# Kernel optimization log

Hardware: AMD Instinct MI355X
Metric: run time of the kernel (lower is better)

The kernel has to match this reference:

```python
import jax, jax.numpy as jnp
import numpy as np

KLD_SCALE = 10.0
COMMIT_COST = 0.25


def setup_inputs() -> dict:
    key = jax.random.key(0)
    k1, k2, k3, k4 = jax.random.split(key, 4)
    B, C, T = 32, 512, 4096
    D, K = 128, 1024
    z = jax.random.normal(k1, (B, C, T), dtype=jnp.float32)
    proj_w = jax.random.normal(k2, (D, C), dtype=jnp.float32) * (1.0 / np.sqrt(C))
    proj_b = jax.random.normal(k3, (D,), dtype=jnp.float32) * 0.01
    embed_w = jax.random.normal(k4, (K, D), dtype=jnp.float32)
    return {"z": z, "proj_w": proj_w, "proj_b": proj_b, "embed_w": embed_w}


def reference(z, proj_w, proj_b, embed_w):
    B, C, T = z.shape
    D = proj_w.shape[0]
    # 1x1 Conv1d == per-timestep linear: [B,C,T] x [D,C] -> [B,T,D]
    z_e = jnp.einsum('bct,dc->btd', z, proj_w) + proj_b
    flat = z_e.reshape(-1, D)  # [B*T, D]
    # squared euclidean distances to codebook: [B*T, K]
    dist = (jnp.sum(flat * flat, axis=1, keepdims=True)
            - 2.0 * (flat @ embed_w.T)
            + jnp.sum(embed_w * embed_w, axis=1)[None, :])
    ind = jnp.argmin(dist, axis=1).reshape(B, T)  # == argmax(-dist)
    z_q = embed_w[ind]  # [B,T,D] codebook gather
    sg = jax.lax.stop_gradient
    diff = KLD_SCALE * (COMMIT_COST * jnp.mean((sg(z_q) - z_e) ** 2)
                        + jnp.mean((z_q - sg(z_e)) ** 2))
    z_q_ste = z_e + sg(z_q - z_e)  # straight-through estimator
    z_q_out = jnp.transpose(z_q_ste, (0, 2, 1))  # [B,D,T]
    return z_q_out, diff, ind
```

## Files before the change

kernel.cpp:

```cpp
#include <hip/hip_runtime.h>

#define B_N 32
#define C_N 512
#define T_N 4096
#define D_N 128
#define K_N 1024
#define N_N (B_N * T_N)

typedef _Float16 f16x8 __attribute__((ext_vector_type(8)));
typedef float    f32x4 __attribute__((ext_vector_type(4)));

#define ZSWZ_OFF 0
#define ESWZ_OFF 67108864
#define ENS_OFF  67895296
#define IND_OFF  67899392
#define PART_OFF 68423680
#define WSWZ_OFF 68431872

#define GLL(g, s) __builtin_amdgcn_global_load_lds( \
    (const __attribute__((address_space(1))) unsigned int*)(g), \
    (__attribute__((address_space(3))) unsigned int*)(s), 16, 0, 0)

__global__ __launch_bounds__(128) void k_eprep(const float* __restrict__ E,
                                               _Float16* __restrict__ eswz,
                                               float* __restrict__ ens) {
  __shared__ float s2[2];
  const int code = blockIdx.x, d = threadIdx.x;
  const float e  = E[(size_t)code * D_N + d];
  const float es = e * 64.f;
  const _Float16 eh = (_Float16)es;
  const _Float16 el = (_Float16)(es - (float)eh);

  float sq = es * es;
  #pragma unroll
  for (int off = 32; off > 0; off >>= 1) sq += __shfl_down(sq, off);
  if ((d & 63) == 0) s2[d >> 6] = sq;
  __syncthreads();
  if (d == 0) ens[code] = s2[0] + s2[1];

  const int kt = code >> 7, mi = (code >> 4) & 7, lrow = code & 15;
  const int lk = (d >> 3) & 3, i = d & 7, cb = d >> 5;
  const size_t tile = (size_t)kt * 12;
  #define PUT(c, v) eswz[(((tile + (c)) * 512 + mi * 64 + lk * 16 + lrow) << 3) + i] = (v)
  PUT(cb, eh);
  PUT(4 + cb, el);
  PUT(8 + cb, eh);
  #undef PUT
}

__global__ __launch_bounds__(256) void k_wprep(const float* __restrict__ W,
                                               _Float16* __restrict__ wswz) {
  const int e = blockIdx.x * 256 + threadIdx.x;
  const int d = e >> 9, c = e & 511;
  const float x = W[d * C_N + c] * 8.f;
  const _Float16 h  = (_Float16)x;
  const _Float16 lo = (_Float16)(x - (float)h);
  const int kc = c >> 5, gg = (c >> 3) & 3, j = c & 7;
  const int nf = d >> 4, ll = gg * 16 + (d & 15);
  const size_t base = (size_t)kc * 8192 + ((size_t)nf * 64 + ll) * 8 + j;
  wswz[base]        = h;
  wswz[base + 4096] = lo;
}

__global__ __launch_bounds__(256, 2) void k_projm(const float* __restrict__ z,
                                                  const _Float16* __restrict__ wswz,
                                                  const float* __restrict__ bias,
                                                  f16x8* __restrict__ zswz) {
  __shared__ __align__(16) char lds[65536];

  const int tid = threadIdx.x;
  const int l   = tid & 63, w = tid >> 6;
  const int g   = l >> 4, li = l & 15;
  const int b   = blockIdx.y, t0 = blockIdx.x * 128;
  const float* zb = z + (size_t)b * C_N * T_N + t0;

  float bs[8];
  #pragma unroll
  for (int nf = 0; nf < 8; ++nf) bs[nf] = bias[nf * 16 + li] * 64.f;

  f32x4 acc[2][8];
  #pragma unroll
  for (int mi = 0; mi < 2; ++mi)
    #pragma unroll
    for (int nf = 0; nf < 8; ++nf) acc[mi][nf] = (f32x4)0.f;

  auto stage = [&](int kc, int buf) {
    char* zdst = lds + buf * 16384;
    char* wdst = lds + 32768 + buf * 16384;
    #pragma unroll
    for (int s = 0; s < 4; ++s) {
      const int q = w * 4 + s;
      const unsigned v = q * 64 + l;
      const unsigned u = v ^ (((v >> 8) & 1) << 2);
      GLL((const char*)zb +
              ((size_t)(kc * 32 + (u >> 5)) * T_N + (size_t)(u & 31) * 4) * 4,
          zdst + q * 1024);
      GLL((const char*)wswz + (size_t)kc * 16384 + q * 1024 + l * 16,
          wdst + q * 1024);
    }
  };

  stage(0, 0);
  __syncthreads();

  int buf = 0;
  for (int kc = 0; kc < 16; ++kc) {
    if (kc + 1 < 16) stage(kc + 1, buf ^ 1);

    const float* zl = (const float*)(lds + buf * 16384);
    const f16x8* wb = (const f16x8*)(lds + 32768 + buf * 16384);

    f16x8 ah[2], al[2];
    #pragma unroll
    for (int mi = 0; mi < 2; ++mi) {
      const int mt = w * 2 + mi;
      const int a0 = (g * 1024 + mt * 16 + li) ^ ((g & 1) << 4);
      #pragma unroll
      for (int j = 0; j < 8; ++j) {
        const float x = zl[a0 + j * 128] * 8.f;
        const _Float16 h = (_Float16)x;
        ah[mi][j] = h;
        al[mi][j] = (_Float16)(x - (float)h);
      }
    }
    f16x8 bh[8], bl[8];
    #pragma unroll
    for (int nf = 0; nf < 8; ++nf) {
      bh[nf] = wb[nf * 64 + l];
      bl[nf] = wb[512 + nf * 64 + l];
    }
    #pragma unroll
    for (int mi = 0; mi < 2; ++mi)
      #pragma unroll
      for (int nf = 0; nf < 8; ++nf) {
        acc[mi][nf] = __builtin_amdgcn_mfma_f32_16x16x32_f16(ah[mi], bh[nf], acc[mi][nf], 0, 0, 0);
        acc[mi][nf] = __builtin_amdgcn_mfma_f32_16x16x32_f16(al[mi], bh[nf], acc[mi][nf], 0, 0, 0);
        acc[mi][nf] = __builtin_amdgcn_mfma_f32_16x16x32_f16(ah[mi], bl[nf], acc[mi][nf], 0, 0, 0);
      }
    __syncthreads();
    buf ^= 1;
  }

  unsigned* cs = (unsigned*)lds;
  const int n0 = b * T_N + t0;
  for (int p = 0; p < 2; ++p) {
    #pragma unroll
    for (int mi = 0; mi < 2; ++mi) {
      const int trow = (w * 2 + mi) * 16 + g * 4;
      #pragma unroll
      for (int nfl = 0; nfl < 4; ++nfl) {
        const int nf = p * 4 + nfl;
        #pragma unroll
        for (int r = 0; r < 4; ++r) {
          const float x = acc[mi][nf][r] + bs[nf];
          const _Float16 h  = (_Float16)x;
          const _Float16 lo = (_Float16)(x - (float)h);
          cs[(trow + r) * 68 + nfl * 16 + li] =
              (unsigned)__builtin_bit_cast(unsigned short, h) |
              ((unsigned)__builtin_bit_cast(unsigned short, lo) << 16);
        }
      }
    }
    __syncthreads();
    #pragma unroll
    for (int i = 0; i < 4; ++i) {
      const int u = i * 256 + tid;
      const int t = u & 127, dc = u >> 7;
      f16x8 vh, vl;
      #pragma unroll
      for (int e = 0; e < 8; ++e) {
        const unsigned vv = cs[t * 68 + dc * 8 + e];
        vh[e] = __builtin_bit_cast(_Float16, (unsigned short)(vv & 0xffff));
        vl[e] = __builtin_bit_cast(_Float16, (unsigned short)(vv >> 16));
      }
      const int n = n0 + t;
      const int cu = p * 2 + (dc >> 2), lk = dc & 3;
      const size_t idx = ((size_t)(n >> 4) * 8 + cu) * 64 + lk * 16 + (n & 15);
      zswz[idx]       = vh;
      zswz[idx + 256] = vl;
    }
    __syncthreads();
  }
}

__global__ __launch_bounds__(256) void k_argmin(const f16x8* __restrict__ zswz,
                                                const f16x8* __restrict__ eswz,
                                                const float* __restrict__ ens,
                                                int* __restrict__ ind,
                                                float* __restrict__ indf) {
  __shared__ f16x8 rows[4096];
  __shared__ f16x8 abuf[2][512];

  const int tid = threadIdx.x;
  const int l   = tid & 63, w = tid >> 6;
  const int wr  = w >> 1, wc = w & 1;
  const int blk = blockIdx.x;

  const char* zsrc = (const char*)zswz + (size_t)blk * 65536;
  #pragma unroll
  for (int s = 0; s < 16; ++s)
    GLL(zsrc + s * 4096 + tid * 16, &rows[s * 256 + w * 64]);

  {
    const char* asrc = (const char*)eswz;
    GLL(asrc + tid * 16,        &abuf[0][w * 64]);
    GLL(asrc + 4096 + tid * 16, &abuf[0][256 + w * 64]);
  }
  __syncthreads();

  float bestd[4];
  int   bestk[4];
  #pragma unroll
  for (int nf = 0; nf < 4; ++nf) { bestd[nf] = 3.4e38f; bestk[nf] = 0; }

  int buf = 0;
  for (int kt = 0; kt < 8; ++kt) {
    f32x4 acc[4][4];
    #pragma unroll
    for (int mi = 0; mi < 4; ++mi)
      #pragma unroll
      for (int nf = 0; nf < 4; ++nf) acc[mi][nf] = (f32x4)0.f;

    for (int c = 0; c < 12; ++c) {
      int nkt = kt, nc = c + 1;
      if (nc == 12) { nc = 0; ++nkt; }
      if (nkt < 8) {
        const char* asrc = (const char*)eswz + ((size_t)(nkt * 12 + nc) * 512) * 16;
        GLL(asrc + tid * 16,        &abuf[buf ^ 1][w * 64]);
        GLL(asrc + 4096 + tid * 16, &abuf[buf ^ 1][256 + w * 64]);
      }
      const int cu = (c < 8) ? (c & 3) : (c - 4);
      f16x8 bfr[4], afr[4];
      #pragma unroll
      for (int nf = 0; nf < 4; ++nf)
        bfr[nf] = rows[((wc * 4 + nf) * 8 + cu) * 64 + l];
      #pragma unroll
      for (int mi = 0; mi < 4; ++mi)
        afr[mi] = abuf[buf][(wr * 4 + mi) * 64 + l];
      #pragma unroll
      for (int mi = 0; mi < 4; ++mi)
        #pragma unroll
        for (int nf = 0; nf < 4; ++nf)
          acc[mi][nf] = __builtin_amdgcn_mfma_f32_16x16x32_f16(
              afr[mi], bfr[nf], acc[mi][nf], 0, 0, 0);
      __syncthreads();
      buf ^= 1;
    }

    #pragma unroll
    for (int mi = 0; mi < 4; ++mi) {
      const int cbase = kt * 128 + wr * 64 + mi * 16 + ((l >> 4) << 2);
      const float4 e4 = *(const float4*)&ens[cbase];
      const float ev[4] = {e4.x, e4.y, e4.z, e4.w};
      #pragma unroll
      for (int r = 0; r < 4; ++r) {
        const int k = cbase + r;
        #pragma unroll
        for (int nf = 0; nf < 4; ++nf) {
          const float dv = ev[r] - 2.0f * acc[mi][nf][r];
          if (dv < bestd[nf]) { bestd[nf] = dv; bestk[nf] = k; }
        }
      }
    }
  }

  float* sd = (float*)&rows[0];
  int*   sk = (int*)((float*)&rows[0] + 256);
  #pragma unroll
  for (int nf = 0; nf < 4; ++nf) {
    float d = bestd[nf]; int k = bestk[nf];
    #pragma unroll
    for (int off = 16; off < 64; off <<= 1) {
      const float od = __shfl_xor(d, off);
      const int   ok = __shfl_xor(k, off);
      if (od < d || (od == d && ok < k)) { d = od; k = ok; }
    }
    if (l < 16) {
      sd[wr * 128 + wc * 64 + nf * 16 + l] = d;
      sk[wr * 128 + wc * 64 + nf * 16 + l] = k;
    }
  }
  __syncthreads();
  if (tid < 128) {
    float d0 = sd[tid], d1 = sd[128 + tid];
    int   k0 = sk[tid], k1 = sk[128 + tid];
    if (d1 < d0 || (d1 == d0 && k1 < k0)) { d0 = d1; k0 = k1; }
    const int n = blk * 128 + tid;
    ind[n]  = k0;
    indf[n] = (float)k0;
  }
}

__global__ __launch_bounds__(256) void k_out(const f16x8* __restrict__ zswz,
                                             const float* __restrict__ E,
                                             const int* __restrict__ ind,
                                             float* __restrict__ out,
                                             float* __restrict__ part) {
  __shared__ float es[64][129];
  __shared__ int   si[64];
  __shared__ float wsum[4];

  const int b   = blockIdx.y;
  const int t0  = blockIdx.x * 64;
  const int tid = threadIdx.x;

  if (tid < 64) si[tid] = ind[b * T_N + t0 + tid];
  __syncthreads();

  float psum = 0.f;
  const int n0 = b * T_N + t0;
  #pragma unroll
  for (int u = tid; u < 1024; u += 256) {
    const int t = u >> 4, db = u & 15;
    const int n = n0 + t;
    const size_t base = ((size_t)(n >> 4) * 8 + (db >> 2)) * 64 + (db & 3) * 16 + (n & 15);
    const f16x8 vh = zswz[base];
    const f16x8 vl = zswz[base + 256];
    const float* ep = &E[(size_t)si[t] * D_N + db * 8];
    const float4 e0 = *(const float4*)ep;
    const float4 e1 = *(const float4*)(ep + 4);
    const float evv[8] = {e0.x, e0.y, e0.z, e0.w, e1.x, e1.y, e1.z, e1.w};
    #pragma unroll
    for (int j = 0; j < 8; ++j) {
      const float zv = ((float)vh[j] + (float)vl[j]) * 0.015625f;
      const float df = evv[j] - zv;
      psum += df * df;
      es[t][db * 8 + j] = evv[j];
    }
  }
  __syncthreads();

  float* ob = out + (size_t)b * D_N * T_N + t0;
  #pragma unroll
  for (int g = tid; g < 8192; g += 256) {
    const int d = g >> 6, t = g & 63;
    ob[(size_t)d * T_N + t] = es[t][d];
  }

  #pragma unroll
  for (int off = 32; off > 0; off >>= 1) psum += __shfl_down(psum, off);
  if ((tid & 63) == 0) wsum[tid >> 6] = psum;
  __syncthreads();
  if (tid == 0)
    part[blockIdx.y * gridDim.x + blockIdx.x] = wsum[0] + wsum[1] + wsum[2] + wsum[3];
}

__global__ __launch_bounds__(256) void k_diff(const float* __restrict__ part,
                                              float* __restrict__ diff_out) {
  __shared__ double wsd[4];
  const int tid = threadIdx.x;
  double s = 0.0;
  for (int i = tid; i < 2048; i += 256) s += (double)part[i];
  #pragma unroll
  for (int off = 32; off > 0; off >>= 1) s += __shfl_down(s, off);
  if ((tid & 63) == 0) wsd[tid >> 6] = s;
  __syncthreads();
  if (tid == 0) {
    const double tot = wsd[0] + wsd[1] + wsd[2] + wsd[3];
    diff_out[0] = (float)(12.5 * tot / (double)((size_t)N_N * D_N));
  }
}

extern "C" void kernel_launch(void* const* d_in, const int* in_sizes, int n_in,
                              void* d_out, int out_size, void* d_ws, size_t ws_size,
                              hipStream_t stream) {
  const float* z    = (const float*)d_in[0];
  const float* W    = (const float*)d_in[1];
  const float* bias = (const float*)d_in[2];
  const float* E    = (const float*)d_in[3];

  float* out = (float*)d_out;
  float* out_q    = out;
  float* out_diff = out + 16777216;
  float* out_ind  = out + 16777217;

  char* ws = (char*)d_ws;
  f16x8*    zswz = (f16x8*)(ws + ZSWZ_OFF);
  _Float16* eswz = (_Float16*)(ws + ESWZ_OFF);
  float*    ens  = (float*)(ws + ENS_OFF);
  int*      ind  = (int*)(ws + IND_OFF);
  float*    part = (float*)(ws + PART_OFF);
  _Float16* wswz = (_Float16*)(ws + WSWZ_OFF);

  k_eprep<<<K_N, 128, 0, stream>>>(E, eswz, ens);
  k_wprep<<<256, 256, 0, stream>>>(W, wswz);
  k_projm<<<dim3(T_N / 128, B_N), 256, 0, stream>>>(z, wswz, bias, zswz);
  k_argmin<<<N_N / 128, 256, 0, stream>>>(zswz, (const f16x8*)eswz, ens, ind, out_ind);
  k_out<<<dim3(T_N / 64, B_N), 256, 0, stream>>>(zswz, E, ind, out_q, part);
  k_diff<<<1, 256, 0, stream>>>(part, out_diff);
}
```

Before: 243.3 us.

## Fuse codebook gather, commitment loss and transposed output into argmin kernel

Removes the separate k_out kernel and the int index buffer. After each argmin block settles its 128 indices, it gathers codebook rows, computes the squared error against the z_e tile still held in LDS, and writes the transposed output straight to global memory. This saves a launch, rereading z_e from global memory, and an index round trip. In exchange, output stores are no longer staged through LDS for coalescing, k_diff now reduces 4096 partials, and launch bounds request 2 blocks per CU.

```diff
diff --git a/kernel.cpp b/kernel.cpp
--- a/kernel.cpp
+++ b/kernel.cpp
@@ -13,9 +13,8 @@
 #define ZSWZ_OFF 0
 #define ESWZ_OFF 67108864
 #define ENS_OFF  67895296
-#define IND_OFF  67899392
-#define PART_OFF 68423680
 #define WSWZ_OFF 68431872
+#define PART_OFF 68694016
 
 #define GLL(g, s) __builtin_amdgcn_global_load_lds( \
     (const __attribute__((address_space(1))) unsigned int*)(g), \
@@ -183,11 +182,44 @@
   }
 }
 
-__global__ __launch_bounds__(256) void k_argmin(const f16x8* __restrict__ zswz,
-                                                const f16x8* __restrict__ eswz,
-                                                const float* __restrict__ ens,
-                                                int* __restrict__ ind,
-                                                float* __restrict__ indf) {
+template<int NF0>
+__device__ __forceinline__ float gather_lds(int wc, int l, const int* skf,
+                                            const float* E, float* ob,
+                                            const f16x8* rows) {
+  float psum = 0.f;
+  #pragma unroll
+  for (int nl = 0; nl < 2; ++nl) {
+    const int nf = NF0 + nl;
+    const int r = wc * 64 + nf * 16 + (l & 15);
+    const int k = skf[r];
+    const float* Er = E + (size_t)k * D_N;
+    #pragma unroll
+    for (int cu = 0; cu < 4; ++cu) {
+      const int d0 = cu * 32 + (l >> 4) * 8;
+      const float4 e0 = *(const float4*)(Er + d0);
+      const float4 e1 = *(const float4*)(Er + d0 + 4);
+      const float ev[8] = {e0.x, e0.y, e0.z, e0.w, e1.x, e1.y, e1.z, e1.w};
+      const f16x8 hi = rows[(((wc * 4 + nf) * 8 + cu) * 64) + l];
+      const f16x8 lo = rows[(((wc * 4 + nf) * 8 + cu + 4) * 64) + l];
+      #pragma unroll
+      for (int j = 0; j < 8; ++j) {
+        const float ze = ((float)hi[j] + (float)lo[j]) * 0.015625f;
+        const float df = ev[j] - ze;
+        psum += df * df;
+        ob[(size_t)(d0 + j) * T_N + r] = ev[j];
+      }
+    }
+  }
+  return psum;
+}
+
+__global__ __launch_bounds__(256, 2) void k_argmin3(const f16x8* __restrict__ zswz,
+                                                    const f16x8* __restrict__ eswz,
+                                                    const float* __restrict__ ens,
+                                                    const float* __restrict__ E,
+                                                    float* __restrict__ out,
+                                                    float* __restrict__ indf,
+                                                    float* __restrict__ part) {
   __shared__ f16x8 rows[4096];
   __shared__ f16x8 abuf[2][512];
 
@@ -264,8 +296,9 @@
     }
   }
 
-  float* sd = (float*)&rows[0];
-  int*   sk = (int*)((float*)&rows[0] + 256);
+  float* sdl = (float*)abuf;
+  int*   skl = (int*)((float*)abuf + 256);
+  int*   skf = (int*)((float*)abuf + 512);
   #pragma unroll
   for (int nf = 0; nf < 4; ++nf) {
     float d = bestd[nf]; int k = bestk[nf];
@@ -276,73 +309,28 @@
       if (od < d || (od == d && ok < k)) { d = od; k = ok; }
     }
     if (l < 16) {
-      sd[wr * 128 + wc * 64 + nf * 16 + l] = d;
-      sk[wr * 128 + wc * 64 + nf * 16 + l] = k;
+      sdl[wr * 128 + wc * 64 + nf * 16 + l] = d;
+      skl[wr * 128 + wc * 64 + nf * 16 + l] = k;
     }
   }
   __syncthreads();
   if (tid < 128) {
-    float d0 = sd[tid], d1 = sd[128 + tid];
-    int   k0 = sk[tid], k1 = sk[128 + tid];
+    float d0 = sdl[tid], d1 = sdl[128 + tid];
+    int   k0 = skl[tid], k1 = skl[128 + tid];
     if (d1 < d0 || (d1 == d0 && k1 < k0)) { d0 = d1; k0 = k1; }
-    const int n = blk * 128 + tid;
-    ind[n]  = k0;
-    indf[n] = (float)k0;
-  }
-}
-
-__global__ __launch_bounds__(256) void k_out(const f16x8* __restrict__ zswz,
-                                             const float* __restrict__ E,
-                                             const int* __restrict__ ind,
-                                             float* __restrict__ out,
-                                             float* __restrict__ part) {
-  __shared__ float es[64][129];
-  __shared__ int   si[64];
-  __shared__ float wsum[4];
-
-  const int b   = blockIdx.y;
-  const int t0  = blockIdx.x * 64;
-  const int tid = threadIdx.x;
-
-  if (tid < 64) si[tid] = ind[b * T_N + t0 + tid];
-  __syncthreads();
-
-  float psum = 0.f;
-  const int n0 = b * T_N + t0;
-  #pragma unroll
-  for (int u = tid; u < 1024; u += 256) {
-    const int t = u >> 4, db = u & 15;
-    const int n = n0 + t;
-    const size_t base = ((size_t)(n >> 4) * 8 + (db >> 2)) * 64 + (db & 3) * 16 + (n & 15);
-    const f16x8 vh = zswz[base];
-    const f16x8 vl = zswz[base + 256];
-    const float* ep = &E[(size_t)si[t] * D_N + db * 8];
-    const float4 e0 = *(const float4*)ep;
-    const float4 e1 = *(const float4*)(ep + 4);
-    const float evv[8] = {e0.x, e0.y, e0.z, e0.w, e1.x, e1.y, e1.z, e1.w};
-    #pragma unroll
-    for (int j = 0; j < 8; ++j) {
-      const float zv = ((float)vh[j] + (float)vl[j]) * 0.015625f;
-      const float df = evv[j] - zv;
-      psum += df * df;
-      es[t][db * 8 + j] = evv[j];
-    }
-  }
-  __syncthreads();
-
-  float* ob = out + (size_t)b * D_N * T_N + t0;
-  #pragma unroll
-  for (int g = tid; g < 8192; g += 256) {
-    const int d = g >> 6, t = g & 63;
-    ob[(size_t)d * T_N + t] = es[t][d];
-  }
-
-  #pragma unroll
-  for (int off = 32; off > 0; off >>= 1) psum += __shfl_down(psum, off);
-  if ((tid & 63) == 0) wsum[tid >> 6] = psum;
-  __syncthreads();
-  if (tid == 0)
-    part[blockIdx.y * gridDim.x + blockIdx.x] = wsum[0] + wsum[1] + wsum[2] + wsum[3];
+    skf[tid] = k0;
+    indf[blk * 128 + tid] = (float)k0;
+  }
+  __syncthreads();
+
+  const int b  = blk >> 5;
+  const int t0 = (blk & 31) << 7;
+  float* ob = out + (size_t)b * (D_N * T_N) + t0;
+  float psum = (wr == 0) ? gather_lds<0>(wc, l, skf, E, ob, rows)
+                         : gather_lds<2>(wc, l, skf, E, ob, rows);
+  #pragma unroll
+  for (int off = 32; off > 0; off >>= 1) psum += __shfl_xor(psum, off);
+  if (l == 0) part[blk * 4 + w] = psum;
 }
 
 __global__ __launch_bounds__(256) void k_diff(const float* __restrict__ part,
@@ -350,7 +338,7 @@
   __shared__ double wsd[4];
   const int tid = threadIdx.x;
   double s = 0.0;
-  for (int i = tid; i < 2048; i += 256) s += (double)part[i];
+  for (int i = tid; i < 4096; i += 256) s += (double)part[i];
   #pragma unroll
   for (int off = 32; off > 0; off >>= 1) s += __shfl_down(s, off);
   if ((tid & 63) == 0) wsd[tid >> 6] = s;
@@ -378,14 +366,13 @@
   f16x8*    zswz = (f16x8*)(ws + ZSWZ_OFF);
   _Float16* eswz = (_Float16*)(ws + ESWZ_OFF);
   float*    ens  = (float*)(ws + ENS_OFF);
-  int*      ind  = (int*)(ws + IND_OFF);
+  _Float16* wswz = (_Float16*)(ws + WSWZ_OFF);
   float*    part = (float*)(ws + PART_OFF);
-  _Float16* wswz = (_Float16*)(ws + WSWZ_OFF);
 
   k_eprep<<<K_N, 128, 0, stream>>>(E, eswz, ens);
   k_wprep<<<256, 256, 0, stream>>>(W, wswz);
   k_projm<<<dim3(T_N / 128, B_N), 256, 0, stream>>>(z, wswz, bias, zswz);
-  k_argmin<<<N_N / 128, 256, 0, stream>>>(zswz, (const f16x8*)eswz, ens, ind, out_ind);
-  k_out<<<dim3(T_N / 64, B_N), 256, 0, stream>>>(zswz, E, ind, out_q, part);
+  k_argmin3<<<N_N / 128, 256, 0, stream>>>(zswz, (const f16x8*)eswz, ens, E,
+                                           out_q, out_ind, part);
   k_diff<<<1, 256, 0, stream>>>(part, out_diff);
 }
```

New measurement: 249.1 us. +2.4%, slower.
